# Kernel tuning notes

Hardware: AMD Instinct MI355X
Metric: run time of the kernel (lower is better)

The kernel has to match this reference:

```python
import jax, jax.numpy as jnp
import numpy as np

D_MODEL = 1024
N_HEADS = 16
D_HEAD = 64
NEG = -1000000000.0


def setup_inputs() -> dict:
    key = jax.random.key(0)
    k1, k2, k3 = jax.random.split(key, 3)
    B, T = 2, 2048
    x = jax.random.normal(k1, (B, T, D_MODEL), dtype=jnp.float32)
    # qkv_proj: Linear(d_model, 3*H*D, bias=False) -> weight (3*H*D, d_model)
    w_qkv = jax.random.normal(k2, (3 * N_HEADS * D_HEAD, D_MODEL), dtype=jnp.float32) * (D_MODEL ** -0.5)
    # o_proj: Linear(H*D, d_model, bias=False) -> weight (d_model, H*D)
    w_o = jax.random.normal(k3, (D_MODEL, N_HEADS * D_HEAD), dtype=jnp.float32) * ((N_HEADS * D_HEAD) ** -0.5)
    return {"x": x, "w_qkv": w_qkv, "w_o": w_o}


def reference(x, w_qkv, w_o):
    B, T, _ = x.shape
    H, D = N_HEADS, D_HEAD
    scale = D ** -0.5
    qkv = jnp.einsum('btm,nm->btn', x, w_qkv).reshape(B, T, 3, H, D)
    q, k, v = qkv[:, :, 0], qkv[:, :, 1], qkv[:, :, 2]  # (B,T,H,D)
    # scores: (B,H,T,T)
    attn = jnp.einsum('bqhd,bkhd->bhqk', q, k) * scale
    causal = jnp.tril(jnp.ones((T, T), dtype=x.dtype))
    attn = attn + (1.0 - causal) * NEG
    attn = jax.nn.softmax(attn, axis=-1)
    out = jnp.einsum('bhqk,bkhd->bqhd', attn, v).reshape(B, T, H * D)
    out = jnp.einsum('btn,mn->btm', out, w_o)
    return (out, k, v)
```

## Files before the change

### kernel.cpp

```cpp
#include <hip/hip_runtime.h>
#include <cstdint>

typedef unsigned short u16;
typedef __bf16 bf16x8 __attribute__((ext_vector_type(8)));
typedef float f32x4 __attribute__((ext_vector_type(4)));
typedef short s4 __attribute__((ext_vector_type(4)));

#define T_SEQ 2048
#define NH 16

__device__ __forceinline__ u16 f2bf(float f) {
  union { float f; uint32_t u; } x; x.f = f;
  uint32_t r = (x.u + 0x7fffu + ((x.u >> 16) & 1u)) >> 16;
  return (u16)r;
}

__device__ __forceinline__ uint32_t pk2bf(float a, float b) {
  union { float f; uint32_t u; } x, y; x.f = a; y.f = b;
  uint32_t lo = (x.u + 0x7fffu + ((x.u >> 16) & 1u)) >> 16;
  uint32_t hi = (y.u + 0x7fffu + ((y.u >> 16) & 1u)) >> 16;
  return lo | (hi << 16);
}

__device__ __forceinline__ void cvt8(u16* dst, const float* src) {
  float4 a = *(const float4*)src;
  float4 b = *(const float4*)(src + 4);
  uint4 o;
  o.x = pk2bf(a.x, a.y); o.y = pk2bf(a.z, a.w);
  o.z = pk2bf(b.x, b.y); o.w = pk2bf(b.z, b.w);
  *(uint4*)dst = o;
}

__global__ __launch_bounds__(256) void cvt_all(const float* __restrict__ x,
                                               const float* __restrict__ wq,
                                               const float* __restrict__ wo,
                                               u16* __restrict__ dst) {
  int i = blockIdx.x * 256 + threadIdx.x;
  const float* src; int off;
  if (i < 524288)      { src = x;  off = 0; }
  else if (i < 917504) { src = wq; off = 524288; }
  else                 { src = wo; off = 917504; }
  cvt8(&dst[(size_t)i * 8], &src[(size_t)(i - off) * 8]);
}

__device__ __forceinline__ s4 cvt4(f32x4 v) {
  union { __bf16 b[4]; s4 s; } u;
  u.b[0] = (__bf16)v[0]; u.b[1] = (__bf16)v[1];
  u.b[2] = (__bf16)v[2]; u.b[3] = (__bf16)v[3];
  return u.s;
}

__device__ __forceinline__ f32x4 mfma16(s4 a, s4 b, f32x4 c) {
#if __has_builtin(__builtin_amdgcn_mfma_f32_16x16x16bf16_1k)
  return __builtin_amdgcn_mfma_f32_16x16x16bf16_1k(a, b, c, 0, 0, 0);
#else
  asm("v_mfma_f32_16x16x16_bf16 %0, %1, %2, %0" : "+v"(c) : "v"(a), "v"(b));
  return c;
#endif
}

__device__ __forceinline__ void gl_lds(const u16* g, u16* ldsbase) {
  __builtin_amdgcn_global_load_lds(
      (const __attribute__((address_space(1))) void*)g,
      (__attribute__((address_space(3))) void*)ldsbase, 16, 0, 0);
}

template <bool CF32, bool KV>
__global__ __launch_bounds__(256) void gemm_bt(
    const u16* __restrict__ A, const u16* __restrict__ W,
    void* __restrict__ Cp, float* __restrict__ outk, float* __restrict__ outv,
    int M, int N, int K) {
  __shared__ __align__(16) u16 As[128 * 64];
  __shared__ __align__(16) u16 Bs[128 * 64];
  const int tid  = threadIdx.x;
  const int n0   = blockIdx.x * 128;
  const int m0   = blockIdx.y * 128;
  const int lane = tid & 63;
  const int wave = tid >> 6;
  const int wm   = (wave >> 1) * 64;
  const int wn   = (wave & 1) * 64;
  const int l15  = lane & 15;
  const int quad = lane >> 4;
  const int srow = lane >> 3;
  const int sc   = lane & 7;

  f32x4 acc[4][4];
#pragma unroll
  for (int i = 0; i < 4; i++)
#pragma unroll
    for (int j = 0; j < 4; j++) acc[i][j] = (f32x4){0.f, 0.f, 0.f, 0.f};

  for (int k0 = 0; k0 < K; k0 += 64) {
    __syncthreads();
#pragma unroll
    for (int i = 0; i < 4; i++) {
      int r0  = (i * 4 + wave) * 8;
      int row = r0 + srow;
      int gc  = (sc ^ (row & 7)) << 3;
      gl_lds(&A[(size_t)(m0 + row) * K + k0 + gc], &As[r0 * 64]);
      gl_lds(&W[(size_t)(n0 + row) * K + k0 + gc], &Bs[r0 * 64]);
    }
    __syncthreads();
#pragma unroll
    for (int kk = 0; kk < 64; kk += 32) {
      bf16x8 af[4], bfr[4];
#pragma unroll
      for (int i = 0; i < 4; i++) {
        int arow = wm + i * 16 + l15;
        af[i] = *(const bf16x8*)((const char*)As + arow * 128 +
                                 ((((kk >> 3) + quad) ^ (arow & 7)) << 4));
      }
#pragma unroll
      for (int j = 0; j < 4; j++) {
        int brow = wn + j * 16 + l15;
        bfr[j] = *(const bf16x8*)((const char*)Bs + brow * 128 +
                                  ((((kk >> 3) + quad) ^ (brow & 7)) << 4));
      }
#pragma unroll
      for (int i = 0; i < 4; i++)
#pragma unroll
        for (int j = 0; j < 4; j++)
          acc[i][j] = __builtin_amdgcn_mfma_f32_16x16x32_bf16(af[i], bfr[j], acc[i][j], 0, 0, 0);
    }
  }
#pragma unroll
  for (int i = 0; i < 4; i++)
#pragma unroll
    for (int j = 0; j < 4; j++)
#pragma unroll
      for (int r = 0; r < 4; r++) {
        int row = m0 + wm + i * 16 + quad * 4 + r;
        int col = n0 + wn + j * 16 + l15;
        float v = acc[i][j][r];
        if constexpr (CF32) {
          ((float*)Cp)[(size_t)row * N + col] = v;
        } else {
          ((u16*)Cp)[(size_t)row * N + col] = f2bf(v);
          if constexpr (KV) {
            if (col >= 2048)      outv[(size_t)row * 1024 + (col - 2048)] = v;
            else if (col >= 1024) outk[(size_t)row * 1024 + (col - 1024)] = v;
          }
        }
      }
}

__global__ __launch_bounds__(256) void transpose_v(const u16* __restrict__ qkv,
                                                   u16* __restrict__ vt) {
  __shared__ __align__(16) u16 tile[64 * 72];
  int t0 = blockIdx.x * 64;
  int bh = blockIdx.y;
  int b = bh >> 4, h = bh & 15;
  int tid = threadIdx.x;
  int t8 = tid & 7, rowb = tid >> 3;
#pragma unroll
  for (int r = 0; r < 2; r++) {
    int row = rowb + r * 32;
    *(uint4*)&tile[row * 72 + t8 * 8] =
        *(const uint4*)&qkv[((size_t)b * T_SEQ + t0 + row) * 3072 + 2048 + h * 64 + t8 * 8];
  }
  __syncthreads();
#pragma unroll
  for (int r = 0; r < 2; r++) {
    int d = rowb + r * 32;
    union { u16 s[8]; uint4 u; } tmp;
#pragma unroll
    for (int e = 0; e < 8; e++) tmp.s[e] = tile[(t8 * 8 + e) * 72 + d];
    *(uint4*)&vt[((size_t)(b * NH + h) * 64 + d) * 2048 + t0 + t8 * 8] = tmp.u;
  }
}

__global__ __launch_bounds__(256) void attn(const u16* __restrict__ qkv,
                                            const u16* __restrict__ vt,
                                            u16* __restrict__ o) {
  __shared__ __align__(16) u16 Ks[2][64 * 64];
  __shared__ __align__(16) u16 Vts[2][64 * 64];

  const int tid  = threadIdx.x;
  const int pair = blockIdx.x;
  const int bh   = blockIdx.y;
  const int b    = bh >> 4, h = bh & 15;
  const int lane = tid & 63, wave = tid >> 6;
  const int l15  = lane & 15, quad = lane >> 4;
  const int srow = lane >> 3, sc = lane & 7;
  const size_t qbase = (size_t)b * T_SEQ * 3072;
  const size_t vbase = (size_t)(b * NH + h) * 64 * 2048;

  const int qtA = pair, qtB = 31 - pair;
  const int wq0A = qtA * 64 + wave * 16;
  const int wq0B = qtB * 64 + wave * 16;
  const u16* qpA = &qkv[qbase + (size_t)(wq0A + l15) * 3072 + h * 64];
  const u16* qpB = &qkv[qbase + (size_t)(wq0B + l15) * 3072 + h * 64];
  bf16x8 qf0 = *(const bf16x8*)&qpA[quad * 8];
  bf16x8 qf1 = *(const bf16x8*)&qpA[32 + quad * 8];
  const bf16x8 qB0 = *(const bf16x8*)&qpB[quad * 8];
  const bf16x8 qB1 = *(const bf16x8*)&qpB[32 + quad * 8];

  int qt = qtA, wq0 = wq0A, qrow = wq0A + l15;

  f32x4 acc_o[4];
#pragma unroll
  for (int n = 0; n < 4; n++) acc_o[n] = (f32x4){0.f, 0.f, 0.f, 0.f};
  float mrun = -1e30f, lrun = 0.f;

  auto stage = [&](int d, int k0) {
#pragma unroll
    for (int i = 0; i < 2; i++) {
      int r0  = (wave * 2 + i) * 8;
      int row = r0 + srow;
      int gc  = (sc ^ (row & 7)) << 3;
      gl_lds(&qkv[qbase + (size_t)(k0 + row) * 3072 + 1024 + h * 64 + gc], &Ks[d][r0 * 64]);
      gl_lds(&vt[vbase + (size_t)row * 2048 + k0 + gc], &Vts[d][r0 * 64]);
    }
  };

  auto writeout = [&]() {
    float linv = 1.0f / lrun;
#pragma unroll
    for (int r = 0; r < 4; r++) {
      float lr = __shfl(linv, quad * 4 + r);
      int row = wq0 + quad * 4 + r;
#pragma unroll
      for (int n = 0; n < 4; n++)
        o[(size_t)(b * T_SEQ + row) * 1024 + h * 64 + n * 16 + l15] =
            f2bf(acc_o[n][r] * lr);
    }
  };

  stage(0, 0);

  const int steps = 33;
  for (int s = 0; s < steps; s++) {
    const int kt = (s > pair) ? (s - pair - 1) : s;
    const int d  = s & 1;

    __syncthreads();

    if (s + 1 < steps) {
      int kt_n = (s + 1 > pair) ? (s - pair) : (s + 1);
      stage(d ^ 1, kt_n * 64);
    }

    if (s == pair + 1) {
      writeout();
#pragma unroll
      for (int n = 0; n < 4; n++) acc_o[n] = (f32x4){0.f, 0.f, 0.f, 0.f};
      mrun = -1e30f; lrun = 0.f;
      qt = qtB; wq0 = wq0B; qrow = wq0B + l15;
      qf0 = qB0; qf1 = qB1;
    }

    const int k0 = kt * 64;

    f32x4 sacc[4];
#pragma unroll
    for (int j = 0; j < 4; j++) sacc[j] = (f32x4){0.f, 0.f, 0.f, 0.f};
#pragma unroll
    for (int j = 0; j < 4; j++) {
      int krow = j * 16 + l15;
      const char* kb = (const char*)&Ks[d][0] + krow * 128;
      bf16x8 kfa = *(const bf16x8*)(kb + ((quad ^ (krow & 7)) << 4));
      bf16x8 kfb = *(const bf16x8*)(kb + (((4 + quad) ^ (krow & 7)) << 4));
      sacc[j] = __builtin_amdgcn_mfma_f32_16x16x32_bf16(kfa, qf0, sacc[j], 0, 0, 0);
      sacc[j] = __builtin_amdgcn_mfma_f32_16x16x32_bf16(kfb, qf1, sacc[j], 0, 0, 0);
    }

    if (kt == qt) {
#pragma unroll
      for (int j = 0; j < 4; j++)
#pragma unroll
        for (int r = 0; r < 4; r++) {
          int k = k0 + j * 16 + quad * 4 + r;
          sacc[j][r] = (k > qrow) ? -1e30f : sacc[j][r] * 0.125f;
        }
    } else {
#pragma unroll
      for (int j = 0; j < 4; j++)
#pragma unroll
        for (int r = 0; r < 4; r++) sacc[j][r] *= 0.125f;
    }

    float mx = sacc[0][0];
#pragma unroll
    for (int j = 0; j < 4; j++)
#pragma unroll
      for (int r = 0; r < 4; r++) mx = fmaxf(mx, sacc[j][r]);
    mx = fmaxf(mx, __shfl_xor(mx, 16));
    mx = fmaxf(mx, __shfl_xor(mx, 32));
    const float mnew  = fmaxf(mrun, mx);
    const float alpha = __expf(mrun - mnew);
    float sum = 0.f;
#pragma unroll
    for (int j = 0; j < 4; j++)
#pragma unroll
      for (int r = 0; r < 4; r++) {
        float p = __expf(sacc[j][r] - mnew);
        sacc[j][r] = p;
        sum += p;
      }
    sum += __shfl_xor(sum, 16);
    sum += __shfl_xor(sum, 32);
    lrun = lrun * alpha + sum;
    mrun = mnew;

#pragma unroll
    for (int r = 0; r < 4; r++) {
      float ar = __shfl(alpha, quad * 4 + r);
#pragma unroll
      for (int n = 0; n < 4; n++) acc_o[n][r] *= ar;
    }

    s4 pa[4];
#pragma unroll
    for (int j = 0; j < 4; j++) pa[j] = cvt4(sacc[j]);

#pragma unroll
    for (int j = 0; j < 4; j++)
#pragma unroll
      for (int n = 0; n < 4; n++) {
        int vrow = n * 16 + l15;
        int ch = (j * 2 + (quad >> 1)) ^ (vrow & 7);
        const s4 vf = *(const s4*)((const char*)&Vts[d][0] + vrow * 128 +
                                   (ch << 4) + ((quad & 1) << 3));
        acc_o[n] = mfma16(pa[j], vf, acc_o[n]);
      }
  }

  writeout();
}

extern "C" void kernel_launch(void* const* d_in, const int* in_sizes, int n_in,
                              void* d_out, int out_size, void* d_ws, size_t ws_size,
                              hipStream_t stream) {
  const float* x     = (const float*)d_in[0];
  const float* w_qkv = (const float*)d_in[1];
  const float* w_o   = (const float*)d_in[2];
  float* out  = (float*)d_out;
  float* outk = out + (size_t)4194304;
  float* outv = out + (size_t)8388608;

  u16* qkv = (u16*)d_ws;
  u16* vt  = qkv + (size_t)4096 * 3072;
  u16* ao  = vt  + (size_t)4194304;
  u16* xb  = ao  + (size_t)4194304;
  u16* wqb = xb  + (size_t)4194304;
  u16* wob = wqb + (size_t)3145728;

  cvt_all<<<4096, 256, 0, stream>>>(x, w_qkv, w_o, xb);

  gemm_bt<false, true><<<dim3(24, 32), 256, 0, stream>>>(
      xb, wqb, qkv, outk, outv, 4096, 3072, 1024);
  transpose_v<<<dim3(32, 32), 256, 0, stream>>>(qkv, vt);
  attn<<<dim3(16, 32), 256, 0, stream>>>(qkv, vt, ao);
  gemm_bt<true, false><<<dim3(8, 32), 256, 0, stream>>>(
      ao, wob, out, nullptr, nullptr, 4096, 1024, 1024);
}
```

Measured before the change: 214.5 us.

## Restructure attention into 8-wave blocks with exp2 softmax and lazy rescaling, swizzle GEMM tiles

The attention kernel now launches 512 threads per block. Two groups of four waves each handle one of two adjacent query tiles and share the K/V tiles staged in LDS, replacing the old sequential pairing of query tile p with 31-p. Softmax uses exp2 with the scale folded into a single FMA, and the running max is rescaled only when any lane's max grows by more than 8 in log2 units, which skips most alpha multiplies. The GEMM remaps block indices with an XCD-style swizzle to improve L2 locality. The trade-off is imbalance: the group working on the earlier tile sits idle for the last step, and blocks now do unequal amounts of work (p varies), so per-block load is less balanced.

```diff
diff --git a/kernel.cpp b/kernel.cpp
--- a/kernel.cpp
+++ b/kernel.cpp
@@ -59,6 +59,14 @@
 #endif
 }
 
+__device__ __forceinline__ float exp2fast(float x) {
+#if __has_builtin(__builtin_amdgcn_exp2f)
+  return __builtin_amdgcn_exp2f(x);
+#else
+  float r; asm("v_exp_f32 %0, %1" : "=v"(r) : "v"(x)); return r;
+#endif
+}
+
 __device__ __forceinline__ void gl_lds(const u16* g, u16* ldsbase) {
   __builtin_amdgcn_global_load_lds(
       (const __attribute__((address_space(1))) void*)g,
@@ -73,8 +81,11 @@
   __shared__ __align__(16) u16 As[128 * 64];
   __shared__ __align__(16) u16 Bs[128 * 64];
   const int tid  = threadIdx.x;
-  const int n0   = blockIdx.x * 128;
-  const int m0   = blockIdx.y * 128;
+  const int bid  = blockIdx.y * gridDim.x + blockIdx.x;
+  const int per  = (gridDim.x * gridDim.y) >> 3;
+  const int swz  = (bid & 7) * per + (bid >> 3);
+  const int n0   = (swz % gridDim.x) * 128;
+  const int m0   = (swz / gridDim.x) * 128;
   const int lane = tid & 63;
   const int wave = tid >> 6;
   const int wm   = (wave >> 1) * 64;
@@ -169,163 +180,143 @@
   }
 }
 
-__global__ __launch_bounds__(256) void attn(const u16* __restrict__ qkv,
+__global__ __launch_bounds__(512) void attn(const u16* __restrict__ qkv,
                                             const u16* __restrict__ vt,
                                             u16* __restrict__ o) {
   __shared__ __align__(16) u16 Ks[2][64 * 64];
   __shared__ __align__(16) u16 Vts[2][64 * 64];
 
   const int tid  = threadIdx.x;
-  const int pair = blockIdx.x;
+  const int p    = 15 - (int)blockIdx.x;
   const int bh   = blockIdx.y;
   const int b    = bh >> 4, h = bh & 15;
   const int lane = tid & 63, wave = tid >> 6;
+  const int grp  = wave >> 2;
+  const int w4   = wave & 3;
   const int l15  = lane & 15, quad = lane >> 4;
   const int srow = lane >> 3, sc = lane & 7;
   const size_t qbase = (size_t)b * T_SEQ * 3072;
   const size_t vbase = (size_t)(b * NH + h) * 64 * 2048;
-
-  const int qtA = pair, qtB = 31 - pair;
-  const int wq0A = qtA * 64 + wave * 16;
-  const int wq0B = qtB * 64 + wave * 16;
-  const u16* qpA = &qkv[qbase + (size_t)(wq0A + l15) * 3072 + h * 64];
-  const u16* qpB = &qkv[qbase + (size_t)(wq0B + l15) * 3072 + h * 64];
-  bf16x8 qf0 = *(const bf16x8*)&qpA[quad * 8];
-  bf16x8 qf1 = *(const bf16x8*)&qpA[32 + quad * 8];
-  const bf16x8 qB0 = *(const bf16x8*)&qpB[quad * 8];
-  const bf16x8 qB1 = *(const bf16x8*)&qpB[32 + quad * 8];
-
-  int qt = qtA, wq0 = wq0A, qrow = wq0A + l15;
+  const float C = 0.1803368801f;
+
+  const int qt   = 2 * p + 1 - grp;
+  const int wq0  = qt * 64 + w4 * 16;
+  const int qrow = wq0 + l15;
+
+  const u16* qp = &qkv[qbase + (size_t)qrow * 3072 + h * 64];
+  const bf16x8 qf0 = *(const bf16x8*)&qp[quad * 8];
+  const bf16x8 qf1 = *(const bf16x8*)&qp[32 + quad * 8];
 
   f32x4 acc_o[4];
 #pragma unroll
   for (int n = 0; n < 4; n++) acc_o[n] = (f32x4){0.f, 0.f, 0.f, 0.f};
-  float mrun = -1e30f, lrun = 0.f;
+  float m2run = -1e30f, lrun = 0.f;
 
   auto stage = [&](int d, int k0) {
-#pragma unroll
-    for (int i = 0; i < 2; i++) {
-      int r0  = (wave * 2 + i) * 8;
-      int row = r0 + srow;
-      int gc  = (sc ^ (row & 7)) << 3;
-      gl_lds(&qkv[qbase + (size_t)(k0 + row) * 3072 + 1024 + h * 64 + gc], &Ks[d][r0 * 64]);
-      gl_lds(&vt[vbase + (size_t)row * 2048 + k0 + gc], &Vts[d][r0 * 64]);
+    int r0  = wave * 8;
+    int row = r0 + srow;
+    int gc  = (sc ^ (row & 7)) << 3;
+    gl_lds(&qkv[qbase + (size_t)(k0 + row) * 3072 + 1024 + h * 64 + gc], &Ks[d][r0 * 64]);
+    gl_lds(&vt[vbase + (size_t)row * 2048 + k0 + gc], &Vts[d][r0 * 64]);
+  };
+
+  stage(0, 0);
+
+  const int steps = 2 * p + 2;
+  for (int s = 0; s < steps; s++) {
+    const int d = s & 1;
+    __syncthreads();
+
+    if (s + 1 < steps) stage(d ^ 1, (s + 1) * 64);
+
+    if (s <= qt) {
+      const int k0 = s * 64;
+
+      f32x4 sacc[4];
+#pragma unroll
+      for (int j = 0; j < 4; j++) sacc[j] = (f32x4){0.f, 0.f, 0.f, 0.f};
+#pragma unroll
+      for (int j = 0; j < 4; j++) {
+        int krow = j * 16 + l15;
+        const char* kb = (const char*)&Ks[d][0] + krow * 128;
+        bf16x8 kfa = *(const bf16x8*)(kb + ((quad ^ (krow & 7)) << 4));
+        bf16x8 kfb = *(const bf16x8*)(kb + (((4 + quad) ^ (krow & 7)) << 4));
+        sacc[j] = __builtin_amdgcn_mfma_f32_16x16x32_bf16(kfa, qf0, sacc[j], 0, 0, 0);
+        sacc[j] = __builtin_amdgcn_mfma_f32_16x16x32_bf16(kfb, qf1, sacc[j], 0, 0, 0);
+      }
+
+      if (s == qt) {
+#pragma unroll
+        for (int j = 0; j < 4; j++)
+#pragma unroll
+          for (int r = 0; r < 4; r++) {
+            int k = k0 + j * 16 + quad * 4 + r;
+            if (k > qrow) sacc[j][r] = -1e30f;
+          }
+      }
+
+      float mj[4];
+#pragma unroll
+      for (int j = 0; j < 4; j++)
+        mj[j] = fmaxf(fmaxf(sacc[j][0], sacc[j][1]), fmaxf(sacc[j][2], sacc[j][3]));
+      float mx = fmaxf(fmaxf(mj[0], mj[1]), fmaxf(mj[2], mj[3]));
+      mx = fmaxf(mx, __shfl_xor(mx, 16));
+      mx = fmaxf(mx, __shfl_xor(mx, 32));
+      const float m2x = mx * C;
+
+      if (!__all(m2x <= m2run + 8.0f)) {
+        const float m2new = fmaxf(m2run, m2x);
+        const float alpha = exp2fast(m2run - m2new);
+        lrun *= alpha;
+        m2run = m2new;
+#pragma unroll
+        for (int r = 0; r < 4; r++) {
+          float ar = __shfl(alpha, quad * 4 + r);
+#pragma unroll
+          for (int n = 0; n < 4; n++) acc_o[n][r] *= ar;
+        }
+      }
+
+      const float nm = m2run;
+      float ts[4];
+#pragma unroll
+      for (int j = 0; j < 4; j++) {
+#pragma unroll
+        for (int r = 0; r < 4; r++) sacc[j][r] = exp2fast(fmaf(sacc[j][r], C, -nm));
+        ts[j] = (sacc[j][0] + sacc[j][1]) + (sacc[j][2] + sacc[j][3]);
+      }
+      float sum = (ts[0] + ts[1]) + (ts[2] + ts[3]);
+      sum += __shfl_xor(sum, 16);
+      sum += __shfl_xor(sum, 32);
+      lrun += sum;
+
+      s4 pa[4];
+#pragma unroll
+      for (int j = 0; j < 4; j++) pa[j] = cvt4(sacc[j]);
+
+#pragma unroll
+      for (int j = 0; j < 4; j++)
+#pragma unroll
+        for (int n = 0; n < 4; n++) {
+          int vrow = n * 16 + l15;
+          int ch = (j * 2 + (quad >> 1)) ^ (vrow & 7);
+          const s4 vf = *(const s4*)((const char*)&Vts[d][0] + vrow * 128 +
+                                     (ch << 4) + ((quad & 1) << 3));
+          acc_o[n] = mfma16(pa[j], vf, acc_o[n]);
+        }
     }
-  };
-
-  auto writeout = [&]() {
-    float linv = 1.0f / lrun;
-#pragma unroll
-    for (int r = 0; r < 4; r++) {
-      float lr = __shfl(linv, quad * 4 + r);
-      int row = wq0 + quad * 4 + r;
-#pragma unroll
-      for (int n = 0; n < 4; n++)
-        o[(size_t)(b * T_SEQ + row) * 1024 + h * 64 + n * 16 + l15] =
-            f2bf(acc_o[n][r] * lr);
-    }
-  };
-
-  stage(0, 0);
-
-  const int steps = 33;
-  for (int s = 0; s < steps; s++) {
-    const int kt = (s > pair) ? (s - pair - 1) : s;
-    const int d  = s & 1;
-
-    __syncthreads();
-
-    if (s + 1 < steps) {
-      int kt_n = (s + 1 > pair) ? (s - pair) : (s + 1);
-      stage(d ^ 1, kt_n * 64);
-    }
-
-    if (s == pair + 1) {
-      writeout();
-#pragma unroll
-      for (int n = 0; n < 4; n++) acc_o[n] = (f32x4){0.f, 0.f, 0.f, 0.f};
-      mrun = -1e30f; lrun = 0.f;
-      qt = qtB; wq0 = wq0B; qrow = wq0B + l15;
-      qf0 = qB0; qf1 = qB1;
-    }
-
-    const int k0 = kt * 64;
-
-    f32x4 sacc[4];
-#pragma unroll
-    for (int j = 0; j < 4; j++) sacc[j] = (f32x4){0.f, 0.f, 0.f, 0.f};
-#pragma unroll
-    for (int j = 0; j < 4; j++) {
-      int krow = j * 16 + l15;
-      const char* kb = (const char*)&Ks[d][0] + krow * 128;
-      bf16x8 kfa = *(const bf16x8*)(kb + ((quad ^ (krow & 7)) << 4));
-      bf16x8 kfb = *(const bf16x8*)(kb + (((4 + quad) ^ (krow & 7)) << 4));
-      sacc[j] = __builtin_amdgcn_mfma_f32_16x16x32_bf16(kfa, qf0, sacc[j], 0, 0, 0);
-      sacc[j] = __builtin_amdgcn_mfma_f32_16x16x32_bf16(kfb, qf1, sacc[j], 0, 0, 0);
-    }
-
-    if (kt == qt) {
-#pragma unroll
-      for (int j = 0; j < 4; j++)
-#pragma unroll
-        for (int r = 0; r < 4; r++) {
-          int k = k0 + j * 16 + quad * 4 + r;
-          sacc[j][r] = (k > qrow) ? -1e30f : sacc[j][r] * 0.125f;
-        }
-    } else {
-#pragma unroll
-      for (int j = 0; j < 4; j++)
-#pragma unroll
-        for (int r = 0; r < 4; r++) sacc[j][r] *= 0.125f;
-    }
-
-    float mx = sacc[0][0];
-#pragma unroll
-    for (int j = 0; j < 4; j++)
-#pragma unroll
-      for (int r = 0; r < 4; r++) mx = fmaxf(mx, sacc[j][r]);
-    mx = fmaxf(mx, __shfl_xor(mx, 16));
-    mx = fmaxf(mx, __shfl_xor(mx, 32));
-    const float mnew  = fmaxf(mrun, mx);
-    const float alpha = __expf(mrun - mnew);
-    float sum = 0.f;
-#pragma unroll
-    for (int j = 0; j < 4; j++)
-#pragma unroll
-      for (int r = 0; r < 4; r++) {
-        float p = __expf(sacc[j][r] - mnew);
-        sacc[j][r] = p;
-        sum += p;
-      }
-    sum += __shfl_xor(sum, 16);
-    sum += __shfl_xor(sum, 32);
-    lrun = lrun * alpha + sum;
-    mrun = mnew;
-
-#pragma unroll
-    for (int r = 0; r < 4; r++) {
-      float ar = __shfl(alpha, quad * 4 + r);
-#pragma unroll
-      for (int n = 0; n < 4; n++) acc_o[n][r] *= ar;
-    }
-
-    s4 pa[4];
-#pragma unroll
-    for (int j = 0; j < 4; j++) pa[j] = cvt4(sacc[j]);
-
-#pragma unroll
-    for (int j = 0; j < 4; j++)
-#pragma unroll
-      for (int n = 0; n < 4; n++) {
-        int vrow = n * 16 + l15;
-        int ch = (j * 2 + (quad >> 1)) ^ (vrow & 7);
-        const s4 vf = *(const s4*)((const char*)&Vts[d][0] + vrow * 128 +
-                                   (ch << 4) + ((quad & 1) << 3));
-        acc_o[n] = mfma16(pa[j], vf, acc_o[n]);
-      }
-  }
-
-  writeout();
+  }
+
+  const float linv = 1.0f / lrun;
+#pragma unroll
+  for (int r = 0; r < 4; r++) {
+    const float lr = __shfl(linv, quad * 4 + r);
+    const int row = wq0 + quad * 4 + r;
+#pragma unroll
+    for (int n = 0; n < 4; n++)
+      o[(size_t)(b * T_SEQ + row) * 1024 + h * 64 + n * 16 + l15] =
+          f2bf(acc_o[n][r] * lr);
+  }
 }
 
 extern "C" void kernel_launch(void* const* d_in, const int* in_sizes, int n_in,
@@ -350,7 +341,7 @@
   gemm_bt<false, true><<<dim3(24, 32), 256, 0, stream>>>(
       xb, wqb, qkv, outk, outv, 4096, 3072, 1024);
   transpose_v<<<dim3(32, 32), 256, 0, stream>>>(qkv, vt);
-  attn<<<dim3(16, 32), 256, 0, stream>>>(qkv, vt, ao);
+  attn<<<dim3(16, 32), 512, 0, stream>>>(qkv, vt, ao);
   gemm_bt<true, false><<<dim3(8, 32), 256, 0, stream>>>(
       ao, wob, out, nullptr, nullptr, 4096, 1024, 1024);
 }
```

New measurement: 226.0 us. 5.3% more time.
